# Kernel optimization log

Hardware: AMD Instinct MI355X
Metric: run time of the kernel (lower is better)

The kernel has to match this reference:

```python
import jax, jax.numpy as jnp
import numpy as np


def _node_layer(X, Z, adj_v, T, W, b, p):
    # d_e = (Z @ p^T): per-edge scalar; multiplier = T diag(d_e) T^T  (Nv,Nv)
    d = (Z @ p.T)[:, 0]
    mult = (T * d[None, :]) @ T.T
    n = mult.shape[0]
    idx = jnp.arange(n)
    M = mult.at[idx, idx].set(1.0)           # diagonal forced to 1
    A = M * adj_v
    A = A / jnp.max(A, axis=0, keepdims=True)  # column-max normalization
    return A @ (X @ W) + b, Z


def _edge_layer(X, Z, adj_e, T, W, b, p):
    # d_v = (X @ p^T): per-node scalar; multiplier = T^T diag(d_v) T  (Ne,Ne)
    d = (X @ p.T)[:, 0]
    mult = (T.T * d[None, :]) @ T
    n = mult.shape[0]
    idx = jnp.arange(n)
    M = mult.at[idx, idx].set(1.0)
    A = M * adj_e
    A = A / jnp.max(A, axis=0, keepdims=True)
    return X, A @ (Z @ W) + b


def setup_inputs() -> dict:
    key = jax.random.key(0)
    ks = jax.random.split(key, 16)
    B, Nv, Ne = 16, 1024, 2048
    Fv, Fe, H, C = 128, 64, 128, 16
    inp = {
        "X": jax.random.normal(ks[0], (B, Nv, Fv), jnp.float32),
        "Z": jax.random.normal(ks[1], (B, Ne, Fe), jnp.float32),
        "adj_e": jax.random.uniform(ks[2], (B, Ne, Ne), jnp.float32, 0.01, 1.0),
        "adj_v": jax.random.uniform(ks[3], (B, Nv, Nv), jnp.float32, 0.01, 1.0),
        "T": jax.random.uniform(ks[4], (B, Nv, Ne), jnp.float32),
        # gc1: node layer  nfeat_v -> nhid, p over edge features
        "W1": jax.random.normal(ks[5], (Fv, H), jnp.float32) * 0.05,
        "b1": jnp.zeros((H,), jnp.float32),
        "p1": jax.random.normal(ks[6], (1, Fe), jnp.float32),
        # gc2: edge layer  nfeat_e -> nfeat_e, p over node features (nhid)
        "W2": jax.random.normal(ks[7], (Fe, Fe), jnp.float32) * 0.05,
        "b2": jnp.zeros((Fe,), jnp.float32),
        "p2": jax.random.normal(ks[8], (1, H), jnp.float32),
        # gc3: node layer  nhid -> nclass
        "W3": jax.random.normal(ks[9], (H, C), jnp.float32) * 0.05,
        "b3": jnp.zeros((C,), jnp.float32),
        "p3": jax.random.normal(ks[10], (1, Fe), jnp.float32),
    }
    return inp


def reference(X, Z, adj_e, adj_v, T, W1, b1, p1, W2, b2, p2, W3, b3, p3):
    # dropout is identity in eval mode
    def single(x, z, ae, av, t):
        x1, z1 = _node_layer(x, z, av, t, W1, b1, p1)
        x1, z1 = jax.nn.relu(x1), jax.nn.relu(z1)
        x2, z2 = _edge_layer(x1, z1, ae, t, W2, b2, p2)
        x2, z2 = jax.nn.relu(x2), jax.nn.relu(z2)
        x3, _ = _node_layer(x2, z2, av, t, W3, b3, p3)
        return x3
    return jax.vmap(single)(X, Z, adj_e, adj_v, T)  # (B, Nv, nclass)
```

## Files before the change

kernel.cpp:

```cpp
#include <hip/hip_runtime.h>
#include <hip/hip_bf16.h>
#include <stdint.h>

#define DEVI __device__ __forceinline__

typedef __bf16 bf16x8_t __attribute__((ext_vector_type(8)));
typedef float f32x4_t __attribute__((ext_vector_type(4)));
typedef unsigned short u16;

static constexpr int NBATCH = 16;
static constexpr int NV = 1024;
static constexpr int NE = 2048;
static constexpr int FV = 128;
static constexpr int FE = 64;
static constexpr int HID = 128;
static constexpr int NCLS = 16;

DEVI u16 f2bf(float f) { __hip_bfloat16 h = __float2bfloat16(f); return *reinterpret_cast<u16*>(&h); }
DEVI float bf2f(u16 u) { union { unsigned int i; float f; } x; x.i = ((unsigned int)u) << 16; return x.f; }

DEVI void gload_lds16(const void* g, void* l) {
  __builtin_amdgcn_global_load_lds(
      (const __attribute__((address_space(1))) unsigned int*)g,
      (__attribute__((address_space(3))) unsigned int*)l, 16, 0, 0);
}

template <bool WRITE_ASC>
__global__ void k_transpose(const float* __restrict__ T, u16* __restrict__ Tbf,
                            u16* __restrict__ Ttbf, const float* __restrict__ d1,
                            u16* __restrict__ Asc1) {
  __shared__ u16 s[32][33];
  const int b = blockIdx.z;
  const int e0 = blockIdx.x * 32, v0 = blockIdx.y * 32;
  const float* Tb = T + (size_t)b * NV * NE;
  u16* T1 = Tbf + (size_t)b * NV * NE;
  u16* T2 = Ttbf + (size_t)b * NE * NV;
  const int tx = threadIdx.x & 31, ty = threadIdx.x >> 5;
  float dv = 0.f;
  if (WRITE_ASC) dv = d1[(size_t)b * NE + e0 + tx];
  #pragma unroll
  for (int i = 0; i < 4; ++i) {
    int v = v0 + ty + i * 8;
    float f = Tb[(size_t)v * NE + e0 + tx];
    u16 u = f2bf(f);
    T1[(size_t)v * NE + e0 + tx] = u;
    if (WRITE_ASC) Asc1[(size_t)b * NV * NE + (size_t)v * NE + e0 + tx] = f2bf(f * dv);
    s[ty + i * 8][tx] = u;
  }
  __syncthreads();
  #pragma unroll
  for (int i = 0; i < 4; ++i) {
    int e = e0 + ty + i * 8;
    T2[(size_t)e * NV + v0 + tx] = s[tx][ty + i * 8];
  }
}

__global__ void k_rowdot(const float* __restrict__ In, const float* __restrict__ p,
                         float* __restrict__ d, int R, int C) {
  const int b = blockIdx.y;
  const int w = threadIdx.x >> 6, l = threadIdx.x & 63;
  const int r = blockIdx.x * 4 + w;
  const float* row = In + ((size_t)b * R + r) * C;
  float s = 0.f;
  for (int c = l; c < C; c += 64) s += row[c] * p[c];
  #pragma unroll
  for (int o = 32; o; o >>= 1) s += __shfl_xor(s, o);
  if (l == 0) d[(size_t)b * R + r] = s;
}

__global__ void k_scale(const u16* __restrict__ In, const float* __restrict__ d,
                        u16* __restrict__ Out, int K, int b0) {
  const int bi = blockIdx.y, bg = b0 + bi;
  const size_t elems = (size_t)NV * NE;
  const size_t idx = ((size_t)blockIdx.x * 256 + threadIdx.x) * 8;
  const float* dd = d + (size_t)bg * K;
  const int k = (int)(idx & (size_t)(K - 1));
  const u16* in = In + (size_t)bg * elems + idx;
  uint4 raw = *(const uint4*)in;
  float f[8];
  f[0] = bf2f(raw.x & 0xffff); f[1] = bf2f(raw.x >> 16);
  f[2] = bf2f(raw.y & 0xffff); f[3] = bf2f(raw.y >> 16);
  f[4] = bf2f(raw.z & 0xffff); f[5] = bf2f(raw.z >> 16);
  f[6] = bf2f(raw.w & 0xffff); f[7] = bf2f(raw.w >> 16);
  u16 o[8];
  #pragma unroll
  for (int t = 0; t < 8; ++t) o[t] = f2bf(f[t] * dd[k + t]);
  *(uint4*)((u16*)Out + (size_t)bi * elems + idx) = *(uint4*)o;
}

__global__ __launch_bounds__(512, 2) void k_gemm256(
    const u16* __restrict__ A, size_t sA, int ldA,
    const u16* __restrict__ Bm, size_t sB, int ldB,
    int M, int K,
    const float* __restrict__ adj, u16* __restrict__ Pout,
    float* __restrict__ pmax, int b0) {
  extern __shared__ __align__(16) char smem[];
  const int gx = gridDim.x, gy = gridDim.y;
  const int total = gx * gy * gridDim.z;
  int orig = blockIdx.x + gx * (blockIdx.y + gy * blockIdx.z);
  const int cpx = total >> 3;
  int swz = (orig & 7) * cpx + (orig >> 3);
  const int bx = swz % gx;
  const int by = (swz / gx) % gy;
  const int bi = swz / (gx * gy);
  const int bg = b0 + bi;

  const u16* Ab = A + (size_t)bi * sA;
  const u16* Bb = Bm + (size_t)bg * sB;
  const int tm = by * 256, tn = bx * 256;
  const int tid = threadIdx.x, wid = tid >> 6, l = tid & 63;
  const int wr = wid >> 2, wc = wid & 3;

  const int srow = tid >> 3;
  const int scol = (((tid & 7) ^ (srow & 7)) << 3);

  const int Lx = (l & 7) << 4;
  const int colb0 = (((l >> 4) << 4)) ^ Lx;
  const int colb1 = (64 + ((l >> 4) << 4)) ^ Lx;
  const int arowb = (wr * 128 + (l & 15)) * 128;
  const int browb = (wc * 64 + (l & 15)) * 128;

  auto stage = [&](int buf, int k0) {
    char* ab = smem + (buf << 16);
    char* bb = ab + 32768;
    #pragma unroll
    for (int ld2 = 0; ld2 < 4; ++ld2) {
      gload_lds16(Ab + (size_t)(tm + ld2 * 64 + srow) * ldA + (k0 + scol),
                  ab + ld2 * 8192 + tid * 16);
      gload_lds16(Bb + (size_t)(tn + ld2 * 64 + srow) * ldB + (k0 + scol),
                  bb + ld2 * 8192 + tid * 16);
    }
  };

  f32x4_t acc[8][4];
  const f32x4_t zv = {0.f, 0.f, 0.f, 0.f};
  #pragma unroll
  for (int m = 0; m < 8; ++m)
    #pragma unroll
    for (int n = 0; n < 4; ++n) acc[m][n] = zv;

  const int NT = K >> 6;
  stage(0, 0);
  __syncthreads();

  for (int kt = 0; kt < NT; ++kt) {
    const int buf = kt & 1;
    if (kt + 1 < NT) stage(buf ^ 1, (kt + 1) << 6);
    char* abase = smem + (buf << 16);
    char* bbase = abase + 32768;
    bf16x8_t af[4][2], bfr[4][2];
    #pragma unroll
    for (int m = 0; m < 4; ++m) {
      af[m][0] = *(const bf16x8_t*)(abase + arowb + m * 2048 + colb0);
      af[m][1] = *(const bf16x8_t*)(abase + arowb + m * 2048 + colb1);
    }
    #pragma unroll
    for (int n = 0; n < 2; ++n) {
      bfr[n][0] = *(const bf16x8_t*)(bbase + browb + n * 2048 + colb0);
      bfr[n][1] = *(const bf16x8_t*)(bbase + browb + n * 2048 + colb1);
    }
    __builtin_amdgcn_s_setprio(1);
    #pragma unroll
    for (int m = 0; m < 4; ++m)
      #pragma unroll
      for (int n = 0; n < 2; ++n)
        #pragma unroll
        for (int kk = 0; kk < 2; ++kk)
          acc[m][n] = __builtin_amdgcn_mfma_f32_16x16x32_bf16(af[m][kk], bfr[n][kk], acc[m][n], 0, 0, 0);
    __builtin_amdgcn_s_setprio(0);
    #pragma unroll
    for (int n = 2; n < 4; ++n) {
      bfr[n][0] = *(const bf16x8_t*)(bbase + browb + n * 2048 + colb0);
      bfr[n][1] = *(const bf16x8_t*)(bbase + browb + n * 2048 + colb1);
    }
    __builtin_amdgcn_s_setprio(1);
    #pragma unroll
    for (int m = 0; m < 4; ++m)
      #pragma unroll
      for (int n = 2; n < 4; ++n)
        #pragma unroll
        for (int kk = 0; kk < 2; ++kk)
          acc[m][n] = __builtin_amdgcn_mfma_f32_16x16x32_bf16(af[m][kk], bfr[n][kk], acc[m][n], 0, 0, 0);
    __builtin_amdgcn_s_setprio(0);
    #pragma unroll
    for (int m = 0; m < 4; ++m) {
      af[m][0] = *(const bf16x8_t*)(abase + arowb + (m + 4) * 2048 + colb0);
      af[m][1] = *(const bf16x8_t*)(abase + arowb + (m + 4) * 2048 + colb1);
    }
    __builtin_amdgcn_s_setprio(1);
    #pragma unroll
    for (int m = 0; m < 4; ++m)
      #pragma unroll
      for (int n = 2; n < 4; ++n)
        #pragma unroll
        for (int kk = 0; kk < 2; ++kk)
          acc[m + 4][n] = __builtin_amdgcn_mfma_f32_16x16x32_bf16(af[m][kk], bfr[n][kk], acc[m + 4][n], 0, 0, 0);
    __builtin_amdgcn_s_setprio(0);
    __builtin_amdgcn_s_setprio(1);
    #pragma unroll
    for (int m = 0; m < 4; ++m)
      #pragma unroll
      for (int n = 0; n < 2; ++n)
        #pragma unroll
        for (int kk = 0; kk < 2; ++kk)
          acc[m + 4][n] = __builtin_amdgcn_mfma_f32_16x16x32_bf16(af[m][kk], bfr[n][kk], acc[m + 4][n], 0, 0, 0);
    __builtin_amdgcn_s_setprio(0);
    __syncthreads();
  }

  const float* adjb = adj + (size_t)bg * M * M;
  u16* Pb = Pout + (size_t)bi * (size_t)M * M;
  float vmax[4] = {0.f, 0.f, 0.f, 0.f};
  #pragma unroll
  for (int m = 0; m < 8; ++m)
    #pragma unroll
    for (int n = 0; n < 4; ++n)
      #pragma unroll
      for (int q = 0; q < 4; ++q) {
        int row = tm + wr * 128 + m * 16 + (l >> 4) * 4 + q;
        int col = tn + wc * 64 + n * 16 + (l & 15);
        float v = acc[m][n][q];
        if (row == col) v = 1.0f;
        v *= adjb[(size_t)row * M + col];
        vmax[n] = fmaxf(vmax[n], v);
        Pb[(size_t)row * M + col] = f2bf(v);
      }
  #pragma unroll
  for (int n = 0; n < 4; ++n) {
    vmax[n] = fmaxf(vmax[n], __shfl_xor(vmax[n], 16));
    vmax[n] = fmaxf(vmax[n], __shfl_xor(vmax[n], 32));
  }
  float* red = (float*)smem;
  if (l < 16) {
    #pragma unroll
    for (int n = 0; n < 4; ++n)
      red[((wr * 4 + wc) * 4 + n) * 16 + l] = vmax[n];
  }
  __syncthreads();
  if (wr == 0 && l < 16) {
    #pragma unroll
    for (int n = 0; n < 4; ++n) {
      float a = red[((0 * 4 + wc) * 4 + n) * 16 + l];
      float b = red[((1 * 4 + wc) * 4 + n) * 16 + l];
      pmax[((size_t)bi * gy + by) * M + tn + wc * 64 + n * 16 + l] = fmaxf(a, b);
    }
  }
}

__global__ void k_colmax2(const float* __restrict__ pmax, float* __restrict__ c,
                          int N, int G, int b0) {
  const int bi = blockIdx.y, bg = b0 + bi;
  const int j = blockIdx.x * 256 + threadIdx.x;
  const float* pb = pmax + (size_t)bi * G * N;
  float m = 0.f;
  for (int g = 0; g < G; ++g) m = fmaxf(m, pb[(size_t)g * N + j]);
  c[(size_t)bg * N + j] = m;
}

template <int EPI>
__global__ __launch_bounds__(256) void k_gemm(
    const u16* __restrict__ A, size_t sA, int ldA,
    const u16* __restrict__ Bm, size_t sB, int ldB,
    int M, int K, int Nrows, int Ncols,
    const float* __restrict__ bias, float* __restrict__ Fout, int b0) {
  __shared__ __align__(16) u16 As[2][128 * 32];
  __shared__ __align__(16) u16 Bs[2][128 * 32];
  const int bi = blockIdx.z, bg = b0 + bi;
  const u16* Ab = A + (size_t)bi * sA;
  const u16* Bb = Bm + (size_t)bg * sB;
  const int tm = blockIdx.y * 128, tn = blockIdx.x * 128;
  const int tid = threadIdx.x, w = tid >> 6, l = tid & 63;
  const int wm = (w >> 1) * 64, wn = (w & 1) * 64;
  const int lr = l & 15, kg = (l >> 4) * 8;
  const int chunk = l & 3;
  int arow[2], brow[2];
  #pragma unroll
  for (int i = 0; i < 2; ++i) {
    int r = (i * 4 + w) * 16 + (l >> 2);
    arow[i] = tm + r;
    int rb = tn + r;
    brow[i] = rb < Nrows ? rb : Nrows - 1;
  }
  f32x4_t acc[4][4];
  const f32x4_t zv = {0.f, 0.f, 0.f, 0.f};
  #pragma unroll
  for (int m = 0; m < 4; ++m)
    #pragma unroll
    for (int n = 0; n < 4; ++n) acc[m][n] = zv;

  auto stage = [&](int buf, int k0) {
    #pragma unroll
    for (int i = 0; i < 2; ++i) {
      gload_lds16(Ab + (size_t)arow[i] * ldA + k0 + chunk * 8,
                  (char*)As[buf] + (i * 4 + w) * 1024);
      gload_lds16(Bb + (size_t)brow[i] * ldB + k0 + chunk * 8,
                  (char*)Bs[buf] + (i * 4 + w) * 1024);
    }
  };

  const int nsteps = K >> 5;
  stage(0, 0);
  __syncthreads();
  for (int s = 0; s < nsteps; ++s) {
    const int cur = s & 1;
    if (s + 1 < nsteps) stage(cur ^ 1, (s + 1) << 5);
    bf16x8_t af[4], bfr[4];
    #pragma unroll
    for (int m = 0; m < 4; ++m) af[m] = *(const bf16x8_t*)&As[cur][(wm + m * 16 + lr) * 32 + kg];
    #pragma unroll
    for (int n = 0; n < 4; ++n) bfr[n] = *(const bf16x8_t*)&Bs[cur][(wn + n * 16 + lr) * 32 + kg];
    #pragma unroll
    for (int m = 0; m < 4; ++m)
      #pragma unroll
      for (int n = 0; n < 4; ++n)
        acc[m][n] = __builtin_amdgcn_mfma_f32_16x16x32_bf16(af[m], bfr[n], acc[m][n], 0, 0, 0);
    __syncthreads();
  }

  float* Ob = Fout + (size_t)bg * M * Ncols;
  #pragma unroll
  for (int m = 0; m < 4; ++m)
    #pragma unroll
    for (int n = 0; n < 4; ++n)
      #pragma unroll
      for (int q = 0; q < 4; ++q) {
        int row = tm + wm + m * 16 + (l >> 4) * 4 + q;
        int col = tn + wn + n * 16 + lr;
        if (col < Ncols) {
          float v = acc[m][n][q] + bias[col];
          if (EPI == 1) v = fmaxf(v, 0.f);
          Ob[(size_t)row * Ncols + col] = v;
        }
      }
}

template <int EPI>
__global__ __launch_bounds__(256) void k_gemmPY(
    const u16* __restrict__ A, size_t sA, int ldA,
    const u16* __restrict__ Bm, size_t sB,
    int M, int K, int Ncols,
    const float* __restrict__ bias, float* __restrict__ Fout, int b0) {
  __shared__ __align__(16) u16 As[2][128 * 32];
  __shared__ __align__(16) u16 Bs[2][64 * 32];
  const int bi = blockIdx.z, bg = b0 + bi;
  const u16* Ab = A + (size_t)bi * sA;
  const u16* Bb = Bm + (size_t)bg * sB;
  const int tm = blockIdx.y * 128;
  const int tid = threadIdx.x, w = tid >> 6, l = tid & 63;
  const int wm = (w >> 1) * 64, wn = (w & 1) * 32;
  const int lr = l & 15, kg = (l >> 4) * 8;
  const int chunk = l & 3;
  int arow[2];
  #pragma unroll
  for (int i = 0; i < 2; ++i) arow[i] = tm + (i * 4 + w) * 16 + (l >> 2);
  const int brow = w * 16 + (l >> 2);

  f32x4_t acc[4][2];
  const f32x4_t zv = {0.f, 0.f, 0.f, 0.f};
  #pragma unroll
  for (int m = 0; m < 4; ++m)
    #pragma unroll
    for (int n = 0; n < 2; ++n) acc[m][n] = zv;

  auto stage = [&](int buf, int k0) {
    #pragma unroll
    for (int i = 0; i < 2; ++i)
      gload_lds16(Ab + (size_t)arow[i] * ldA + k0 + chunk * 8,
                  (char*)As[buf] + (i * 4 + w) * 1024);
    gload_lds16(Bb + (size_t)brow * ldA  + k0 + chunk * 8,
                (char*)Bs[buf] + tid * 16);
  };

  const int nsteps = K >> 5;
  stage(0, 0);
  __syncthreads();
  for (int s = 0; s < nsteps; ++s) {
    const int cur = s & 1;
    if (s + 1 < nsteps) stage(cur ^ 1, (s + 1) << 5);
    bf16x8_t af[4], bfr[2];
    #pragma unroll
    for (int m = 0; m < 4; ++m) af[m] = *(const bf16x8_t*)&As[cur][(wm + m * 16 + lr) * 32 + kg];
    #pragma unroll
    for (int n = 0; n < 2; ++n) bfr[n] = *(const bf16x8_t*)&Bs[cur][(wn + n * 16 + lr) * 32 + kg];
    #pragma unroll
    for (int m = 0; m < 4; ++m)
      #pragma unroll
      for (int n = 0; n < 2; ++n)
        acc[m][n] = __builtin_amdgcn_mfma_f32_16x16x32_bf16(af[m], bfr[n], acc[m][n], 0, 0, 0);
    __syncthreads();
  }

  float* Ob = Fout + (size_t)bg * M * Ncols;
  #pragma unroll
  for (int m = 0; m < 4; ++m)
    #pragma unroll
    for (int n = 0; n < 2; ++n)
      #pragma unroll
      for (int q = 0; q < 4; ++q) {
        int row = tm + wm + m * 16 + (l >> 4) * 4 + q;
        int col = wn + n * 16 + lr;
        if (col < Ncols) {
          float v = acc[m][n][q] + bias[col];
          if (EPI == 1) v = fmaxf(v, 0.f);
          Ob[(size_t)row * Ncols + col] = v;
        }
      }
}

template <bool RELU_IN>
__global__ __launch_bounds__(256) void k_smallgemm(
    const float* __restrict__ X, size_t sX, int Kd,
    const float* __restrict__ W, int Cc,
    const float* __restrict__ cmax, u16* __restrict__ YT, size_t sY,
    int Nj, int b0) {
  __shared__ float Xs[64][129];
  __shared__ float Ws[128][33];
  const int bg = b0 + blockIdx.y;
  const float* Xb = X + (size_t)bg * sX;
  const int j0 = blockIdx.x * 64;
  const int tid = threadIdx.x;
  for (int idx = tid; idx < 64 * (Kd / 4); idx += 256) {
    int r = idx / (Kd / 4), q = idx % (Kd / 4);
    float4 v = *(const float4*)(Xb + (size_t)(j0 + r) * Kd + q * 4);
    if (RELU_IN) {
      v.x = fmaxf(v.x, 0.f); v.y = fmaxf(v.y, 0.f);
      v.z = fmaxf(v.z, 0.f); v.w = fmaxf(v.w, 0.f);
    }
    Xs[r][q * 4 + 0] = v.x; Xs[r][q * 4 + 1] = v.y;
    Xs[r][q * 4 + 2] = v.z; Xs[r][q * 4 + 3] = v.w;
  }
  const int r = tid & 63, cg = tid >> 6;
  const float rinv = 1.0f / cmax[(size_t)bg * Nj + j0 + r];
  for (int c0 = 0; c0 < Cc; c0 += 32) {
    __syncthreads();
    for (int idx = tid; idx < Kd * 32; idx += 256) {
      int k = idx >> 5, c = c0 + (idx & 31);
      Ws[k][idx & 31] = (c < Cc) ? W[(size_t)k * Cc + c] : 0.f;
    }
    __syncthreads();
    float acc[8] = {0.f, 0.f, 0.f, 0.f, 0.f, 0.f, 0.f, 0.f};
    for (int k = 0; k < Kd; ++k) {
      float xv = Xs[r][k];
      #pragma unroll
      for (int cc = 0; cc < 8; ++cc) acc[cc] += xv * Ws[k][cg * 8 + cc];
    }
    #pragma unroll
    for (int cc = 0; cc < 8; ++cc) {
      int c = c0 + cg * 8 + cc;
      if (c < Cc) YT[(size_t)bg * sY + (size_t)c * Nj + j0 + r] = f2bf(acc[cc] * rinv);
    }
  }
}

extern "C" void kernel_launch(void* const* d_in, const int* in_sizes, int n_in,
                              void* d_out, int out_size, void* d_ws, size_t ws_size,
                              hipStream_t stream) {
  const float* X    = (const float*)d_in[0];
  const float* Z    = (const float*)d_in[1];
  const float* adje = (const float*)d_in[2];
  const float* adjv = (const float*)d_in[3];
  const float* T    = (const float*)d_in[4];
  const float* W1   = (const float*)d_in[5];
  const float* b1   = (const float*)d_in[6];
  const float* p1   = (const float*)d_in[7];
  const float* W2   = (const float*)d_in[8];
  const float* b2   = (const float*)d_in[9];
  const float* p2   = (const float*)d_in[10];
  const float* W3   = (const float*)d_in[11];
  const float* b3   = (const float*)d_in[12];
  const float* p3   = (const float*)d_in[13];
  float* out = (float*)d_out;
  (void)in_sizes; (void)n_in; (void)out_size;

  hipFuncSetAttribute(reinterpret_cast<const void*>(k_gemm256),
                      hipFuncAttributeMaxDynamicSharedMemorySize, 131072);

  char* ws = (char*)d_ws;
  size_t off = 0;
  auto alloc = [&](size_t n) -> char* {
    char* p = ws + off; off = (off + n + 255) & ~(size_t)255; return p;
  };
  u16* Tbf    = (u16*)alloc((size_t)NBATCH * NV * NE * 2);
  u16* Ttbf   = (u16*)alloc((size_t)NBATCH * NE * NV * 2);
  float* dbuf = (float*)alloc((size_t)NBATCH * NE * 4);
  float* cbuf = (float*)alloc((size_t)NBATCH * NE * 4);
  float* pmax = (float*)alloc((size_t)NBATCH * 8 * NE * 4);
  u16* YT     = (u16*)alloc((size_t)NBATCH * NE * 64 * 2);
  float* x1   = (float*)alloc((size_t)NBATCH * NV * HID * 4);
  float* z2   = (float*)alloc((size_t)NBATCH * NE * FE * 4);
  const size_t needA = (size_t)NBATCH * NV * NE * 2;
  const size_t needP = (size_t)NBATCH * NE * NE * 2;
  const bool full = (ws_size >= off + needA + needP + 1024);
  const int nb = full ? NBATCH : 1;
  u16* Asc = (u16*)alloc(full ? needA : (size_t)NV * NE * 2);
  u16* P   = (u16*)alloc(full ? needP : (size_t)NE * NE * 2);

  const dim3 blk(256, 1, 1);
  const dim3 blk512(512, 1, 1);

  k_rowdot<<<dim3(NE / 4, NBATCH), blk, 0, stream>>>(Z, p1, dbuf, NE, FE);
  if (full)
    k_transpose<true><<<dim3(NE / 32, NV / 32, NBATCH), blk, 0, stream>>>(
        T, Tbf, Ttbf, dbuf, Asc);
  else
    k_transpose<false><<<dim3(NE / 32, NV / 32, NBATCH), blk, 0, stream>>>(
        T, Tbf, Ttbf, nullptr, nullptr);

  for (int b0 = 0; b0 < NBATCH; b0 += nb) {
    if (!full)
      k_scale<<<dim3((NV * NE) / 2048, nb), blk, 0, stream>>>(Tbf, dbuf, Asc, NE, b0);
    k_gemm256<<<dim3(NV / 256, NV / 256, nb), blk512, 131072, stream>>>(
        Asc, (size_t)NV * NE, NE, Tbf, (size_t)NV * NE, NE, NV, NE, adjv, P, pmax, b0);
    k_colmax2<<<dim3(NV / 256, nb), blk, 0, stream>>>(pmax, cbuf, NV, NV / 256, b0);
    k_smallgemm<false><<<dim3(NV / 64, nb), blk, 0, stream>>>(
        X, (size_t)NV * FV, FV, W1, HID, cbuf, YT, (size_t)NV * HID, NV, b0);
    k_gemm<1><<<dim3(1, NV / 128, nb), blk, 0, stream>>>(
        P, (size_t)NV * NV, NV, YT, (size_t)NV * HID, NV,
        NV, NV, HID, HID, b1, x1, b0);
  }
  k_rowdot<<<dim3(NV / 4, NBATCH), blk, 0, stream>>>(x1, p2, dbuf, NV, HID);
  for (int b0 = 0; b0 < NBATCH; b0 += nb) {
    k_scale<<<dim3((NE * NV) / 2048, nb), blk, 0, stream>>>(Ttbf, dbuf, Asc, NV, b0);
    k_gemm256<<<dim3(NE / 256, NE / 256, nb), blk512, 131072, stream>>>(
        Asc, (size_t)NE * NV, NV, Ttbf, (size_t)NE * NV, NV, NE, NV, adje, P, pmax, b0);
    k_colmax2<<<dim3(NE / 256, nb), blk, 0, stream>>>(pmax, cbuf, NE, NE / 256, b0);
    k_smallgemm<true><<<dim3(NE / 64, nb), blk, 0, stream>>>(
        Z, (size_t)NE * FE, FE, W2, FE, cbuf, YT, (size_t)NE * FE, NE, b0);
    k_gemmPY<1><<<dim3(1, NE / 128, nb), blk, 0, stream>>>(
        P, (size_t)NE * NE, NE, YT, (size_t)NE * FE,
        NE, NE, FE, b2, z2, b0);
  }
  k_rowdot<<<dim3(NE / 4, NBATCH), blk, 0, stream>>>(z2, p3, dbuf, NE, FE);
  for (int b0 = 0; b0 < NBATCH; b0 += nb) {
    k_scale<<<dim3((NV * NE) / 2048, nb), blk, 0, stream>>>(Tbf, dbuf, Asc, NE, b0);
    k_gemm256<<<dim3(NV / 256, NV / 256, nb), blk512, 131072, stream>>>(
        Asc, (size_t)NV * NE, NE, Tbf, (size_t)NV * NE, NE, NV, NE, adjv, P, pmax, b0);
    k_colmax2<<<dim3(NV / 256, nb), blk, 0, stream>>>(pmax, cbuf, NV, NV / 256, b0);
    k_smallgemm<false><<<dim3(NV / 64, nb), blk, 0, stream>>>(
        x1, (size_t)NV * HID, HID, W3, NCLS, cbuf, YT, (size_t)NV * NCLS, NV, b0);
    k_gemmPY<2><<<dim3(1, NV / 128, nb), blk, 0, stream>>>(
        P, (size_t)NV * NV, NV, YT, (size_t)NV * NCLS,
        NV, NV, NCLS, b3, out, b0);
  }
}
```

Before: 659.7 us.

## Shrink multiplier GEMM to 128x128 tiles and reuse gemmPY for P@Y

Replaces the 256x256-tile, 512-thread multiplier GEMM with a 128x128-tile, 256-thread version that uses half the LDS and issues four times as many blocks. The goal is better CU occupancy and load balance on the 1024-sized node GEMMs, which produced only 16 blocks per batch. The per-tile column-max partials double, so the pmax buffer and colmax reduction count grow. It also drops the generic k_gemm and routes the first-layer P@Y product through k_gemmPY, which gains a column-block offset so it can cover 128 output columns across two blocks. Smaller tiles give less operand reuse per block and more global and L2 traffic.

```diff
diff --git a/kernel.cpp b/kernel.cpp
--- a/kernel.cpp
+++ b/kernel.cpp
@@ -88,7 +88,7 @@
   *(uint4*)((u16*)Out + (size_t)bi * elems + idx) = *(uint4*)o;
 }
 
-__global__ __launch_bounds__(512, 2) void k_gemm256(
+__global__ __launch_bounds__(256, 2) void k_gemm128(
     const u16* __restrict__ A, size_t sA, int ldA,
     const u16* __restrict__ Bm, size_t sB, int ldB,
     int M, int K,
@@ -107,9 +107,10 @@
 
   const u16* Ab = A + (size_t)bi * sA;
   const u16* Bb = Bm + (size_t)bg * sB;
-  const int tm = by * 256, tn = bx * 256;
+  const int tm = by * 128, tn = bx * 128;
   const int tid = threadIdx.x, wid = tid >> 6, l = tid & 63;
-  const int wr = wid >> 2, wc = wid & 3;
+  const int wr = wid >> 1, wc = wid & 1;
+  const int lr = l & 15;
 
   const int srow = tid >> 3;
   const int scol = (((tid & 7) ^ (srow & 7)) << 3);
@@ -117,25 +118,25 @@
   const int Lx = (l & 7) << 4;
   const int colb0 = (((l >> 4) << 4)) ^ Lx;
   const int colb1 = (64 + ((l >> 4) << 4)) ^ Lx;
-  const int arowb = (wr * 128 + (l & 15)) * 128;
-  const int browb = (wc * 64 + (l & 15)) * 128;
+  const int arowb = (wr * 64 + lr) * 128;
+  const int browb = (wc * 64 + lr) * 128;
 
   auto stage = [&](int buf, int k0) {
-    char* ab = smem + (buf << 16);
-    char* bb = ab + 32768;
-    #pragma unroll
-    for (int ld2 = 0; ld2 < 4; ++ld2) {
-      gload_lds16(Ab + (size_t)(tm + ld2 * 64 + srow) * ldA + (k0 + scol),
-                  ab + ld2 * 8192 + tid * 16);
-      gload_lds16(Bb + (size_t)(tn + ld2 * 64 + srow) * ldB + (k0 + scol),
-                  bb + ld2 * 8192 + tid * 16);
+    char* ab = smem + (buf << 15);
+    char* bb = ab + 16384;
+    #pragma unroll
+    for (int i = 0; i < 4; ++i) {
+      gload_lds16(Ab + (size_t)(tm + i * 32 + srow) * ldA + (k0 + scol),
+                  ab + i * 4096 + tid * 16);
+      gload_lds16(Bb + (size_t)(tn + i * 32 + srow) * ldB + (k0 + scol),
+                  bb + i * 4096 + tid * 16);
     }
   };
 
-  f32x4_t acc[8][4];
+  f32x4_t acc[4][4];
   const f32x4_t zv = {0.f, 0.f, 0.f, 0.f};
   #pragma unroll
-  for (int m = 0; m < 8; ++m)
+  for (int m = 0; m < 4; ++m)
     #pragma unroll
     for (int n = 0; n < 4; ++n) acc[m][n] = zv;
 
@@ -146,9 +147,9 @@
   for (int kt = 0; kt < NT; ++kt) {
     const int buf = kt & 1;
     if (kt + 1 < NT) stage(buf ^ 1, (kt + 1) << 6);
-    char* abase = smem + (buf << 16);
-    char* bbase = abase + 32768;
-    bf16x8_t af[4][2], bfr[4][2];
+    char* abase = smem + (buf << 15);
+    char* bbase = abase + 16384;
+    bf16x8_t af[4][2], blo[2][2], bhi[2][2];
     #pragma unroll
     for (int m = 0; m < 4; ++m) {
       af[m][0] = *(const bf16x8_t*)(abase + arowb + m * 2048 + colb0);
@@ -156,8 +157,8 @@
     }
     #pragma unroll
     for (int n = 0; n < 2; ++n) {
-      bfr[n][0] = *(const bf16x8_t*)(bbase + browb + n * 2048 + colb0);
-      bfr[n][1] = *(const bf16x8_t*)(bbase + browb + n * 2048 + colb1);
+      blo[n][0] = *(const bf16x8_t*)(bbase + browb + n * 2048 + colb0);
+      blo[n][1] = *(const bf16x8_t*)(bbase + browb + n * 2048 + colb1);
     }
     __builtin_amdgcn_s_setprio(1);
     #pragma unroll
@@ -166,36 +167,13 @@
       for (int n = 0; n < 2; ++n)
         #pragma unroll
         for (int kk = 0; kk < 2; ++kk)
-          acc[m][n] = __builtin_amdgcn_mfma_f32_16x16x32_bf16(af[m][kk], bfr[n][kk], acc[m][n], 0, 0, 0);
+          acc[m][n] = __builtin_amdgcn_mfma_f32_16x16x32_bf16(af[m][kk], blo[n][kk], acc[m][n], 0, 0, 0);
     __builtin_amdgcn_s_setprio(0);
     #pragma unroll
-    for (int n = 2; n < 4; ++n) {
-      bfr[n][0] = *(const bf16x8_t*)(bbase + browb + n * 2048 + colb0);
-      bfr[n][1] = *(const bf16x8_t*)(bbase + browb + n * 2048 + colb1);
-    }
-    __builtin_amdgcn_s_setprio(1);
-    #pragma unroll
-    for (int m = 0; m < 4; ++m)
-      #pragma unroll
-      for (int n = 2; n < 4; ++n)
-        #pragma unroll
-        for (int kk = 0; kk < 2; ++kk)
-          acc[m][n] = __builtin_amdgcn_mfma_f32_16x16x32_bf16(af[m][kk], bfr[n][kk], acc[m][n], 0, 0, 0);
-    __builtin_amdgcn_s_setprio(0);
-    #pragma unroll
-    for (int m = 0; m < 4; ++m) {
-      af[m][0] = *(const bf16x8_t*)(abase + arowb + (m + 4) * 2048 + colb0);
-      af[m][1] = *(const bf16x8_t*)(abase + arowb + (m + 4) * 2048 + colb1);
-    }
-    __builtin_amdgcn_s_setprio(1);
-    #pragma unroll
-    for (int m = 0; m < 4; ++m)
-      #pragma unroll
-      for (int n = 2; n < 4; ++n)
-        #pragma unroll
-        for (int kk = 0; kk < 2; ++kk)
-          acc[m + 4][n] = __builtin_amdgcn_mfma_f32_16x16x32_bf16(af[m][kk], bfr[n][kk], acc[m + 4][n], 0, 0, 0);
-    __builtin_amdgcn_s_setprio(0);
+    for (int n = 0; n < 2; ++n) {
+      bhi[n][0] = *(const bf16x8_t*)(bbase + browb + (n + 2) * 2048 + colb0);
+      bhi[n][1] = *(const bf16x8_t*)(bbase + browb + (n + 2) * 2048 + colb1);
+    }
     __builtin_amdgcn_s_setprio(1);
     #pragma unroll
     for (int m = 0; m < 4; ++m)
@@ -203,7 +181,7 @@
       for (int n = 0; n < 2; ++n)
         #pragma unroll
         for (int kk = 0; kk < 2; ++kk)
-          acc[m + 4][n] = __builtin_amdgcn_mfma_f32_16x16x32_bf16(af[m][kk], bfr[n][kk], acc[m + 4][n], 0, 0, 0);
+          acc[m][n + 2] = __builtin_amdgcn_mfma_f32_16x16x32_bf16(af[m][kk], bhi[n][kk], acc[m][n + 2], 0, 0, 0);
     __builtin_amdgcn_s_setprio(0);
     __syncthreads();
   }
@@ -212,13 +190,13 @@
   u16* Pb = Pout + (size_t)bi * (size_t)M * M;
   float vmax[4] = {0.f, 0.f, 0.f, 0.f};
   #pragma unroll
-  for (int m = 0; m < 8; ++m)
+  for (int m = 0; m < 4; ++m)
     #pragma unroll
     for (int n = 0; n < 4; ++n)
       #pragma unroll
       for (int q = 0; q < 4; ++q) {
-        int row = tm + wr * 128 + m * 16 + (l >> 4) * 4 + q;
-        int col = tn + wc * 64 + n * 16 + (l & 15);
+        int row = tm + wr * 64 + m * 16 + (l >> 4) * 4 + q;
+        int col = tn + wc * 64 + n * 16 + lr;
         float v = acc[m][n][q];
         if (row == col) v = 1.0f;
         v *= adjb[(size_t)row * M + col];
@@ -234,14 +212,14 @@
   if (l < 16) {
     #pragma unroll
     for (int n = 0; n < 4; ++n)
-      red[((wr * 4 + wc) * 4 + n) * 16 + l] = vmax[n];
+      red[(wid * 4 + n) * 16 + l] = vmax[n];
   }
   __syncthreads();
   if (wr == 0 && l < 16) {
     #pragma unroll
     for (int n = 0; n < 4; ++n) {
-      float a = red[((0 * 4 + wc) * 4 + n) * 16 + l];
-      float b = red[((1 * 4 + wc) * 4 + n) * 16 + l];
+      float a = red[(wid * 4 + n) * 16 + l];
+      float b = red[((wid + 2) * 4 + n) * 16 + l];
       pmax[((size_t)bi * gy + by) * M + tn + wc * 64 + n * 16 + l] = fmaxf(a, b);
     }
   }
@@ -255,83 +233,6 @@
   float m = 0.f;
   for (int g = 0; g < G; ++g) m = fmaxf(m, pb[(size_t)g * N + j]);
   c[(size_t)bg * N + j] = m;
-}
-
-template <int EPI>
-__global__ __launch_bounds__(256) void k_gemm(
-    const u16* __restrict__ A, size_t sA, int ldA,
-    const u16* __restrict__ Bm, size_t sB, int ldB,
-    int M, int K, int Nrows, int Ncols,
-    const float* __restrict__ bias, float* __restrict__ Fout, int b0) {
-  __shared__ __align__(16) u16 As[2][128 * 32];
-  __shared__ __align__(16) u16 Bs[2][128 * 32];
-  const int bi = blockIdx.z, bg = b0 + bi;
-  const u16* Ab = A + (size_t)bi * sA;
-  const u16* Bb = Bm + (size_t)bg * sB;
-  const int tm = blockIdx.y * 128, tn = blockIdx.x * 128;
-  const int tid = threadIdx.x, w = tid >> 6, l = tid & 63;
-  const int wm = (w >> 1) * 64, wn = (w & 1) * 64;
-  const int lr = l & 15, kg = (l >> 4) * 8;
-  const int chunk = l & 3;
-  int arow[2], brow[2];
-  #pragma unroll
-  for (int i = 0; i < 2; ++i) {
-    int r = (i * 4 + w) * 16 + (l >> 2);
-    arow[i] = tm + r;
-    int rb = tn + r;
-    brow[i] = rb < Nrows ? rb : Nrows - 1;
-  }
-  f32x4_t acc[4][4];
-  const f32x4_t zv = {0.f, 0.f, 0.f, 0.f};
-  #pragma unroll
-  for (int m = 0; m < 4; ++m)
-    #pragma unroll
-    for (int n = 0; n < 4; ++n) acc[m][n] = zv;
-
-  auto stage = [&](int buf, int k0) {
-    #pragma unroll
-    for (int i = 0; i < 2; ++i) {
-      gload_lds16(Ab + (size_t)arow[i] * ldA + k0 + chunk * 8,
-                  (char*)As[buf] + (i * 4 + w) * 1024);
-      gload_lds16(Bb + (size_t)brow[i] * ldB + k0 + chunk * 8,
-                  (char*)Bs[buf] + (i * 4 + w) * 1024);
-    }
-  };
-
-  const int nsteps = K >> 5;
-  stage(0, 0);
-  __syncthreads();
-  for (int s = 0; s < nsteps; ++s) {
-    const int cur = s & 1;
-    if (s + 1 < nsteps) stage(cur ^ 1, (s + 1) << 5);
-    bf16x8_t af[4], bfr[4];
-    #pragma unroll
-    for (int m = 0; m < 4; ++m) af[m] = *(const bf16x8_t*)&As[cur][(wm + m * 16 + lr) * 32 + kg];
-    #pragma unroll
-    for (int n = 0; n < 4; ++n) bfr[n] = *(const bf16x8_t*)&Bs[cur][(wn + n * 16 + lr) * 32 + kg];
-    #pragma unroll
-    for (int m = 0; m < 4; ++m)
-      #pragma unroll
-      for (int n = 0; n < 4; ++n)
-        acc[m][n] = __builtin_amdgcn_mfma_f32_16x16x32_bf16(af[m], bfr[n], acc[m][n], 0, 0, 0);
-    __syncthreads();
-  }
-
-  float* Ob = Fout + (size_t)bg * M * Ncols;
-  #pragma unroll
-  for (int m = 0; m < 4; ++m)
-    #pragma unroll
-    for (int n = 0; n < 4; ++n)
-      #pragma unroll
-      for (int q = 0; q < 4; ++q) {
-        int row = tm + wm + m * 16 + (l >> 4) * 4 + q;
-        int col = tn + wn + n * 16 + lr;
-        if (col < Ncols) {
-          float v = acc[m][n][q] + bias[col];
-          if (EPI == 1) v = fmaxf(v, 0.f);
-          Ob[(size_t)row * Ncols + col] = v;
-        }
-      }
 }
 
 template <int EPI>
@@ -346,6 +247,7 @@
   const u16* Ab = A + (size_t)bi * sA;
   const u16* Bb = Bm + (size_t)bg * sB;
   const int tm = blockIdx.y * 128;
+  const int cbase = blockIdx.x * 64;
   const int tid = threadIdx.x, w = tid >> 6, l = tid & 63;
   const int wm = (w >> 1) * 64, wn = (w & 1) * 32;
   const int lr = l & 15, kg = (l >> 4) * 8;
@@ -353,7 +255,8 @@
   int arow[2];
   #pragma unroll
   for (int i = 0; i < 2; ++i) arow[i] = tm + (i * 4 + w) * 16 + (l >> 2);
-  const int brow = w * 16 + (l >> 2);
+  int brow = cbase + w * 16 + (l >> 2);
+  if (brow >= Ncols) brow = Ncols - 1;
 
   f32x4_t acc[4][2];
   const f32x4_t zv = {0.f, 0.f, 0.f, 0.f};
@@ -398,7 +301,7 @@
       #pragma unroll
       for (int q = 0; q < 4; ++q) {
         int row = tm + wm + m * 16 + (l >> 4) * 4 + q;
-        int col = wn + n * 16 + lr;
+        int col = cbase + wn + n * 16 + lr;
         if (col < Ncols) {
           float v = acc[m][n][q] + bias[col];
           if (EPI == 1) v = fmaxf(v, 0.f);
@@ -472,8 +375,8 @@
   float* out = (float*)d_out;
   (void)in_sizes; (void)n_in; (void)out_size;
 
-  hipFuncSetAttribute(reinterpret_cast<const void*>(k_gemm256),
-                      hipFuncAttributeMaxDynamicSharedMemorySize, 131072);
+  hipFuncSetAttribute(reinterpret_cast<const void*>(k_gemm128),
+                      hipFuncAttributeMaxDynamicSharedMemorySize, 65536);
 
   char* ws = (char*)d_ws;
   size_t off = 0;
@@ -484,7 +387,7 @@
   u16* Ttbf   = (u16*)alloc((size_t)NBATCH * NE * NV * 2);
   float* dbuf = (float*)alloc((size_t)NBATCH * NE * 4);
   float* cbuf = (float*)alloc((size_t)NBATCH * NE * 4);
-  float* pmax = (float*)alloc((size_t)NBATCH * 8 * NE * 4);
+  float* pmax = (float*)alloc((size_t)NBATCH * 16 * NE * 4);
   u16* YT     = (u16*)alloc((size_t)NBATCH * NE * 64 * 2);
   float* x1   = (float*)alloc((size_t)NBATCH * NV * HID * 4);
   float* z2   = (float*)alloc((size_t)NBATCH * NE * FE * 4);
@@ -496,7 +399,6 @@
   u16* P   = (u16*)alloc(full ? needP : (size_t)NE * NE * 2);
 
   const dim3 blk(256, 1, 1);
-  const dim3 blk512(512, 1, 1);
 
   k_rowdot<<<dim3(NE / 4, NBATCH), blk, 0, stream>>>(Z, p1, dbuf, NE, FE);
   if (full)
@@ -509,21 +411,21 @@
   for (int b0 = 0; b0 < NBATCH; b0 += nb) {
     if (!full)
       k_scale<<<dim3((NV * NE) / 2048, nb), blk, 0, stream>>>(Tbf, dbuf, Asc, NE, b0);
-    k_gemm256<<<dim3(NV / 256, NV / 256, nb), blk512, 131072, stream>>>(
+    k_gemm128<<<dim3(NV / 128, NV / 128, nb), blk, 65536, stream>>>(
         Asc, (size_t)NV * NE, NE, Tbf, (size_t)NV * NE, NE, NV, NE, adjv, P, pmax, b0);
-    k_colmax2<<<dim3(NV / 256, nb), blk, 0, stream>>>(pmax, cbuf, NV, NV / 256, b0);
+    k_colmax2<<<dim3(NV / 256, nb), blk, 0, stream>>>(pmax, cbuf, NV, NV / 128, b0);
     k_smallgemm<false><<<dim3(NV / 64, nb), blk, 0, stream>>>(
         X, (size_t)NV * FV, FV, W1, HID, cbuf, YT, (size_t)NV * HID, NV, b0);
-    k_gemm<1><<<dim3(1, NV / 128, nb), blk, 0, stream>>>(
-        P, (size_t)NV * NV, NV, YT, (size_t)NV * HID, NV,
-        NV, NV, HID, HID, b1, x1, b0);
+    k_gemmPY<1><<<dim3(2, NV / 128, nb), blk, 0, stream>>>(
+        P, (size_t)NV * NV, NV, YT, (size_t)NV * HID,
+        NV, NV, HID, b1, x1, b0);
   }
   k_rowdot<<<dim3(NV / 4, NBATCH), blk, 0, stream>>>(x1, p2, dbuf, NV, HID);
   for (int b0 = 0; b0 < NBATCH; b0 += nb) {
     k_scale<<<dim3((NE * NV) / 2048, nb), blk, 0, stream>>>(Ttbf, dbuf, Asc, NV, b0);
-    k_gemm256<<<dim3(NE / 256, NE / 256, nb), blk512, 131072, stream>>>(
+    k_gemm128<<<dim3(NE / 128, NE / 128, nb), blk, 65536, stream>>>(
         Asc, (size_t)NE * NV, NV, Ttbf, (size_t)NE * NV, NV, NE, NV, adje, P, pmax, b0);
-    k_colmax2<<<dim3(NE / 256, nb), blk, 0, stream>>>(pmax, cbuf, NE, NE / 256, b0);
+    k_colmax2<<<dim3(NE / 256, nb), blk, 0, stream>>>(pmax, cbuf, NE, NE / 128, b0);
     k_smallgemm<true><<<dim3(NE / 64, nb), blk, 0, stream>>>(
         Z, (size_t)NE * FE, FE, W2, FE, cbuf, YT, (size_t)NE * FE, NE, b0);
     k_gemmPY<1><<<dim3(1, NE / 128, nb), blk, 0, stream>>>(
@@ -533,9 +435,9 @@
   k_rowdot<<<dim3(NE / 4, NBATCH), blk, 0, stream>>>(z2, p3, dbuf, NE, FE);
   for (int b0 = 0; b0 < NBATCH; b0 += nb) {
     k_scale<<<dim3((NV * NE) / 2048, nb), blk, 0, stream>>>(Tbf, dbuf, Asc, NE, b0);
-    k_gemm256<<<dim3(NV / 256, NV / 256, nb), blk512, 131072, stream>>>(
+    k_gemm128<<<dim3(NV / 128, NV / 128, nb), blk, 65536, stream>>>(
         Asc, (size_t)NV * NE, NE, Tbf, (size_t)NV * NE, NE, NV, NE, adjv, P, pmax, b0);
-    k_colmax2<<<dim3(NV / 256, nb), blk, 0, stream>>>(pmax, cbuf, NV, NV / 256, b0);
+    k_colmax2<<<dim3(NV / 256, nb), blk, 0, stream>>>(pmax, cbuf, NV, NV / 128, b0);
     k_smallgemm<false><<<dim3(NV / 64, nb), blk, 0, stream>>>(
         x1, (size_t)NV * HID, HID, W3, NCLS, cbuf, YT, (size_t)NV * NCLS, NV, b0);
     k_gemmPY<2><<<dim3(1, NV / 128, nb), blk, 0, stream>>>(
```

Result: slower. 691.4 us (+4.8%).

## Fuse diagonal scaling of T into the big GEMM A-fragment loads

Applied to the files above, without the earlier changes.

Removes the separate k_scale pass (and the fused Asc write in the transpose) that materialized a scaled bf16 copy of T per layer. The GEMM now reads T for both operands and scales A fragments by the per-k vector d in registers after loading from LDS. This drops a full read and write of a large bf16 tensor per layer and frees workspace. In exchange it adds per-iteration global loads of d and bf16 unpack/multiply/repack ALU work in the MFMA inner loop, which may cost matrix-core throughput.

```diff
diff --git a/kernel.cpp b/kernel.cpp
--- a/kernel.cpp
+++ b/kernel.cpp
@@ -25,10 +25,17 @@
       (__attribute__((address_space(3))) unsigned int*)l, 16, 0, 0);
 }
 
-template <bool WRITE_ASC>
+DEVI bf16x8_t scale8(bf16x8_t v, const float* dk) {
+  union U { bf16x8_t v; u16 s[8]; };
+  U in; in.v = v;
+  U out;
+  #pragma unroll
+  for (int j = 0; j < 8; ++j) out.s[j] = f2bf(bf2f(in.s[j]) * dk[j]);
+  return out.v;
+}
+
 __global__ void k_transpose(const float* __restrict__ T, u16* __restrict__ Tbf,
-                            u16* __restrict__ Ttbf, const float* __restrict__ d1,
-                            u16* __restrict__ Asc1) {
+                            u16* __restrict__ Ttbf) {
   __shared__ u16 s[32][33];
   const int b = blockIdx.z;
   const int e0 = blockIdx.x * 32, v0 = blockIdx.y * 32;
@@ -36,15 +43,11 @@
   u16* T1 = Tbf + (size_t)b * NV * NE;
   u16* T2 = Ttbf + (size_t)b * NE * NV;
   const int tx = threadIdx.x & 31, ty = threadIdx.x >> 5;
-  float dv = 0.f;
-  if (WRITE_ASC) dv = d1[(size_t)b * NE + e0 + tx];
   #pragma unroll
   for (int i = 0; i < 4; ++i) {
     int v = v0 + ty + i * 8;
-    float f = Tb[(size_t)v * NE + e0 + tx];
-    u16 u = f2bf(f);
+    u16 u = f2bf(Tb[(size_t)v * NE + e0 + tx]);
     T1[(size_t)v * NE + e0 + tx] = u;
-    if (WRITE_ASC) Asc1[(size_t)b * NV * NE + (size_t)v * NE + e0 + tx] = f2bf(f * dv);
     s[ty + i * 8][tx] = u;
   }
   __syncthreads();
@@ -68,30 +71,9 @@
   if (l == 0) d[(size_t)b * R + r] = s;
 }
 
-__global__ void k_scale(const u16* __restrict__ In, const float* __restrict__ d,
-                        u16* __restrict__ Out, int K, int b0) {
-  const int bi = blockIdx.y, bg = b0 + bi;
-  const size_t elems = (size_t)NV * NE;
-  const size_t idx = ((size_t)blockIdx.x * 256 + threadIdx.x) * 8;
-  const float* dd = d + (size_t)bg * K;
-  const int k = (int)(idx & (size_t)(K - 1));
-  const u16* in = In + (size_t)bg * elems + idx;
-  uint4 raw = *(const uint4*)in;
-  float f[8];
-  f[0] = bf2f(raw.x & 0xffff); f[1] = bf2f(raw.x >> 16);
-  f[2] = bf2f(raw.y & 0xffff); f[3] = bf2f(raw.y >> 16);
-  f[4] = bf2f(raw.z & 0xffff); f[5] = bf2f(raw.z >> 16);
-  f[6] = bf2f(raw.w & 0xffff); f[7] = bf2f(raw.w >> 16);
-  u16 o[8];
-  #pragma unroll
-  for (int t = 0; t < 8; ++t) o[t] = f2bf(f[t] * dd[k + t]);
-  *(uint4*)((u16*)Out + (size_t)bi * elems + idx) = *(uint4*)o;
-}
-
 __global__ __launch_bounds__(512, 2) void k_gemm256(
-    const u16* __restrict__ A, size_t sA, int ldA,
-    const u16* __restrict__ Bm, size_t sB, int ldB,
-    int M, int K,
+    const u16* __restrict__ Tm, size_t sT, int ld,
+    const float* __restrict__ dvec, int M, int K,
     const float* __restrict__ adj, u16* __restrict__ Pout,
     float* __restrict__ pmax, int b0) {
   extern __shared__ __align__(16) char smem[];
@@ -105,8 +87,8 @@
   const int bi = swz / (gx * gy);
   const int bg = b0 + bi;
 
-  const u16* Ab = A + (size_t)bi * sA;
-  const u16* Bb = Bm + (size_t)bg * sB;
+  const u16* Tb = Tm + (size_t)bg * sT;
+  const float* dK = dvec + (size_t)bg * K;
   const int tm = by * 256, tn = bx * 256;
   const int tid = threadIdx.x, wid = tid >> 6, l = tid & 63;
   const int wr = wid >> 2, wc = wid & 3;
@@ -119,16 +101,17 @@
   const int colb1 = (64 + ((l >> 4) << 4)) ^ Lx;
   const int arowb = (wr * 128 + (l & 15)) * 128;
   const int browb = (wc * 64 + (l & 15)) * 128;
+  const int kf = (l >> 4) << 3;
 
   auto stage = [&](int buf, int k0) {
     char* ab = smem + (buf << 16);
     char* bb = ab + 32768;
     #pragma unroll
-    for (int ld2 = 0; ld2 < 4; ++ld2) {
-      gload_lds16(Ab + (size_t)(tm + ld2 * 64 + srow) * ldA + (k0 + scol),
-                  ab + ld2 * 8192 + tid * 16);
-      gload_lds16(Bb + (size_t)(tn + ld2 * 64 + srow) * ldB + (k0 + scol),
-                  bb + ld2 * 8192 + tid * 16);
+    for (int i = 0; i < 4; ++i) {
+      gload_lds16(Tb + (size_t)(tm + i * 64 + srow) * ld + (k0 + scol),
+                  ab + i * 8192 + tid * 16);
+      gload_lds16(Tb + (size_t)(tn + i * 64 + srow) * ld + (k0 + scol),
+                  bb + i * 8192 + tid * 16);
     }
   };
 
@@ -145,14 +128,24 @@
 
   for (int kt = 0; kt < NT; ++kt) {
     const int buf = kt & 1;
+    const int k0 = kt << 6;
     if (kt + 1 < NT) stage(buf ^ 1, (kt + 1) << 6);
+    float dk0[8], dk1[8];
+    {
+      f32x4_t a = *(const f32x4_t*)(dK + k0 + kf);
+      f32x4_t b = *(const f32x4_t*)(dK + k0 + kf + 4);
+      f32x4_t c = *(const f32x4_t*)(dK + k0 + 32 + kf);
+      f32x4_t e = *(const f32x4_t*)(dK + k0 + 32 + kf + 4);
+      #pragma unroll
+      for (int j = 0; j < 4; ++j) { dk0[j] = a[j]; dk0[j + 4] = b[j]; dk1[j] = c[j]; dk1[j + 4] = e[j]; }
+    }
     char* abase = smem + (buf << 16);
     char* bbase = abase + 32768;
     bf16x8_t af[4][2], bfr[4][2];
     #pragma unroll
     for (int m = 0; m < 4; ++m) {
-      af[m][0] = *(const bf16x8_t*)(abase + arowb + m * 2048 + colb0);
-      af[m][1] = *(const bf16x8_t*)(abase + arowb + m * 2048 + colb1);
+      af[m][0] = scale8(*(const bf16x8_t*)(abase + arowb + m * 2048 + colb0), dk0);
+      af[m][1] = scale8(*(const bf16x8_t*)(abase + arowb + m * 2048 + colb1), dk1);
     }
     #pragma unroll
     for (int n = 0; n < 2; ++n) {
@@ -184,8 +177,8 @@
     __builtin_amdgcn_s_setprio(0);
     #pragma unroll
     for (int m = 0; m < 4; ++m) {
-      af[m][0] = *(const bf16x8_t*)(abase + arowb + (m + 4) * 2048 + colb0);
-      af[m][1] = *(const bf16x8_t*)(abase + arowb + (m + 4) * 2048 + colb1);
+      af[m][0] = scale8(*(const bf16x8_t*)(abase + arowb + (m + 4) * 2048 + colb0), dk0);
+      af[m][1] = scale8(*(const bf16x8_t*)(abase + arowb + (m + 4) * 2048 + colb1), dk1);
     }
     __builtin_amdgcn_s_setprio(1);
     #pragma unroll
@@ -488,29 +481,20 @@
   u16* YT     = (u16*)alloc((size_t)NBATCH * NE * 64 * 2);
   float* x1   = (float*)alloc((size_t)NBATCH * NV * HID * 4);
   float* z2   = (float*)alloc((size_t)NBATCH * NE * FE * 4);
-  const size_t needA = (size_t)NBATCH * NV * NE * 2;
   const size_t needP = (size_t)NBATCH * NE * NE * 2;
-  const bool full = (ws_size >= off + needA + needP + 1024);
+  const bool full = (ws_size >= off + needP + 1024);
   const int nb = full ? NBATCH : 1;
-  u16* Asc = (u16*)alloc(full ? needA : (size_t)NV * NE * 2);
-  u16* P   = (u16*)alloc(full ? needP : (size_t)NE * NE * 2);
+  u16* P = (u16*)alloc(full ? needP : (size_t)NE * NE * 2);
 
   const dim3 blk(256, 1, 1);
   const dim3 blk512(512, 1, 1);
 
   k_rowdot<<<dim3(NE / 4, NBATCH), blk, 0, stream>>>(Z, p1, dbuf, NE, FE);
-  if (full)
-    k_transpose<true><<<dim3(NE / 32, NV / 32, NBATCH), blk, 0, stream>>>(
-        T, Tbf, Ttbf, dbuf, Asc);
-  else
-    k_transpose<false><<<dim3(NE / 32, NV / 32, NBATCH), blk, 0, stream>>>(
-        T, Tbf, Ttbf, nullptr, nullptr);
+  k_transpose<<<dim3(NE / 32, NV / 32, NBATCH), blk, 0, stream>>>(T, Tbf, Ttbf);
 
   for (int b0 = 0; b0 < NBATCH; b0 += nb) {
-    if (!full)
-      k_scale<<<dim3((NV * NE) / 2048, nb), blk, 0, stream>>>(Tbf, dbuf, Asc, NE, b0);
     k_gemm256<<<dim3(NV / 256, NV / 256, nb), blk512, 131072, stream>>>(
-        Asc, (size_t)NV * NE, NE, Tbf, (size_t)NV * NE, NE, NV, NE, adjv, P, pmax, b0);
+        Tbf, (size_t)NV * NE, NE, dbuf, NV, NE, adjv, P, pmax, b0);
     k_colmax2<<<dim3(NV / 256, nb), blk, 0, stream>>>(pmax, cbuf, NV, NV / 256, b0);
     k_smallgemm<false><<<dim3(NV / 64, nb), blk, 0, stream>>>(
         X, (size_t)NV * FV, FV, W1, HID, cbuf, YT, (size_t)NV * HID, NV, b0);
@@ -520,9 +504,8 @@
   }
   k_rowdot<<<dim3(NV / 4, NBATCH), blk, 0, stream>>>(x1, p2, dbuf, NV, HID);
   for (int b0 = 0; b0 < NBATCH; b0 += nb) {
-    k_scale<<<dim3((NE * NV) / 2048, nb), blk, 0, stream>>>(Ttbf, dbuf, Asc, NV, b0);
     k_gemm256<<<dim3(NE / 256, NE / 256, nb), blk512, 131072, stream>>>(
-        Asc, (size_t)NE * NV, NV, Ttbf, (size_t)NE * NV, NV, NE, NV, adje, P, pmax, b0);
+        Ttbf, (size_t)NE * NV, NV, dbuf, NE, NV, adje, P, pmax, b0);
     k_colmax2<<<dim3(NE / 256, nb), blk, 0, stream>>>(pmax, cbuf, NE, NE / 256, b0);
     k_smallgemm<true><<<dim3(NE / 64, nb), blk, 0, stream>>>(
         Z, (size_t)NE * FE, FE, W2, FE, cbuf, YT, (size_t)NE * FE, NE, b0);
@@ -532,9 +515,8 @@
   }
   k_rowdot<<<dim3(NE / 4, NBATCH), blk, 0, stream>>>(z2, p3, dbuf, NE, FE);
   for (int b0 = 0; b0 < NBATCH; b0 += nb) {
-    k_scale<<<dim3((NV * NE) / 2048, nb), blk, 0, stream>>>(Tbf, dbuf, Asc, NE, b0);
     k_gemm256<<<dim3(NV / 256, NV / 256, nb), blk512, 131072, stream>>>(
-        Asc, (size_t)NV * NE, NE, Tbf, (size_t)NV * NE, NE, NV, NE, adjv, P, pmax, b0);
+        Tbf, (size_t)NV * NE, NE, dbuf, NV, NE, adjv, P, pmax, b0);
     k_colmax2<<<dim3(NV / 256, nb), blk, 0, stream>>>(pmax, cbuf, NV, NV / 256, b0);
     k_smallgemm<false><<<dim3(NV / 64, nb), blk, 0, stream>>>(
         x1, (size_t)NV * HID, HID, W3, NCLS, cbuf, YT, (size_t)NV * NCLS, NV, b0);
```

After: 740.5 us. 1.12x slower.
